# Optimization experiments

Hardware: AMD Instinct MI355X
Metric: run time of the kernel (lower is better)

Reference implementation:

```python
import jax, jax.numpy as jnp
import numpy as np

EMB_DIM = 1024
N_HEADS = 16
HEAD_DIM = EMB_DIM // N_HEADS
MAX_SEQ_LEN = 2048
THETA = 10000.0
B, T = 2, 2048


def _precompute_rope(head_dim, max_seq_len, theta=THETA):
    freqs = 1.0 / theta ** (np.arange(0, head_dim, 2, dtype=np.float32) / head_dim)
    t = np.arange(max_seq_len, dtype=np.float32)
    ang = np.outer(t, freqs)  # [T, D/2]
    return jnp.asarray(np.cos(ang)), jnp.asarray(np.sin(ang))


def setup_inputs() -> dict:
    key = jax.random.key(0)
    kx, kqkv, kp, kb = jax.random.split(key, 4)
    x = jax.random.normal(kx, (B, T, EMB_DIM), dtype=jnp.float32)
    # nn.Linear weights stored as [out, in]; we keep [in, out] for x @ W
    s1 = 1.0 / np.sqrt(EMB_DIM)
    Wqkv = jax.random.uniform(kqkv, (EMB_DIM, 3 * EMB_DIM), minval=-s1, maxval=s1, dtype=jnp.float32)
    Wproj = jax.random.uniform(kp, (EMB_DIM, EMB_DIM), minval=-s1, maxval=s1, dtype=jnp.float32)
    bproj = jax.random.uniform(kb, (EMB_DIM,), minval=-s1, maxval=s1, dtype=jnp.float32)
    cos, sin = _precompute_rope(HEAD_DIM, MAX_SEQ_LEN)
    return {"x": x, "Wqkv": Wqkv, "Wproj": Wproj, "bproj": bproj, "cos": cos, "sin": sin}


def _apply_rope(x, cos, sin):
    # x: [B,H,T,D]; cos/sin: [max_T, D/2]
    T_ = x.shape[-2]
    c, s = cos[:T_], sin[:T_]  # [T, D/2], broadcasts over B,H
    xe, xo = x[..., ::2], x[..., 1::2]
    re = xe * c - xo * s
    ro = xe * s + xo * c
    return jnp.stack([re, ro], axis=-1).reshape(x.shape)


def reference(x, Wqkv, Wproj, bproj, cos, sin):
    Bq, Tq, C = x.shape
    qkv = x @ Wqkv  # [B,T,3C]
    q, k, v = jnp.split(qkv, 3, axis=-1)
    def to_heads(t):
        return t.reshape(Bq, Tq, N_HEADS, HEAD_DIM).transpose(0, 2, 1, 3)  # [B,H,T,D]
    q, k, v = to_heads(q), to_heads(k), to_heads(v)
    q = _apply_rope(q, cos, sin)
    k = _apply_rope(k, cos, sin)
    scale = 1.0 / jnp.sqrt(jnp.asarray(HEAD_DIM, dtype=x.dtype))
    scores = jnp.einsum('bhqd,bhkd->bhqk', q, k) * scale  # [B,H,T,T]
    causal = jnp.tril(jnp.ones((Tq, Tq), dtype=bool))
    scores = jnp.where(causal, scores, jnp.asarray(-jnp.inf, dtype=scores.dtype))
    attn = jax.nn.softmax(scores, axis=-1)
    out = jnp.einsum('bhqk,bhkd->bhqd', attn, v)  # [B,H,T,D]
    out = out.transpose(0, 2, 1, 3).reshape(Bq, Tq, C)
    return out @ Wproj + bproj
```

## Files before the change

kernel.cpp:

```cpp
#include <hip/hip_runtime.h>

typedef __attribute__((ext_vector_type(8))) short short8;
typedef __attribute__((ext_vector_type(4))) float f32x4;
typedef __attribute__((ext_vector_type(4))) unsigned short u16x4;
typedef unsigned short ushort_t;

#define GLOAD16(gp, sp) __builtin_amdgcn_global_load_lds( \
    (const __attribute__((address_space(1))) void*)(gp),  \
    (__attribute__((address_space(3))) void*)(sp), 16, 0, 0)

#define MFMA(a, b, c) __builtin_amdgcn_mfma_f32_16x16x32_bf16(a, b, c, 0, 0, 0)

__device__ __forceinline__ ushort_t f2b(float f) {
    union { float f; unsigned u; } c; c.f = f;
    unsigned r = (c.u + 0x7FFFu + ((c.u >> 16) & 1u)) >> 16;
    return (ushort_t)r;
}
__device__ __forceinline__ float b2f(ushort_t u) {
    union { unsigned u; float f; } c; c.u = ((unsigned)u) << 16;
    return c.f;
}

__global__ void cvt_bf16(const float* __restrict__ in, ushort_t* __restrict__ out, int n) {
    int i = (blockIdx.x * 256 + threadIdx.x) * 4;
    if (i < n) {
        f32x4 v = *(const f32x4*)(in + i);
        u16x4 o;
        #pragma unroll
        for (int j = 0; j < 4; j++) o[j] = f2b(v[j]);
        *(u16x4*)(out + i) = o;
    }
}

__global__ __launch_bounds__(256) void transpose_cvt(const float* __restrict__ in,
                                                     ushort_t* __restrict__ out,
                                                     int R, int Cc) {
    __shared__ float tile[32][33];
    int tx = threadIdx.x & 31, ty = threadIdx.x >> 5;
    int c0 = blockIdx.x * 32, r0 = blockIdx.y * 32;
    #pragma unroll
    for (int i = 0; i < 32; i += 8)
        tile[ty + i][tx] = in[(size_t)(r0 + ty + i) * Cc + c0 + tx];
    __syncthreads();
    #pragma unroll
    for (int i = 0; i < 32; i += 8)
        out[(size_t)(c0 + ty + i) * R + r0 + tx] = f2b(tile[tx][ty + i]);
}

template <bool F32OUT, bool BIAS>
__global__ __launch_bounds__(256) void gemm_bt(const ushort_t* __restrict__ A,
                                               const ushort_t* __restrict__ Bt,
                                               void* __restrict__ Cout,
                                               const float* __restrict__ bias,
                                               int M, int N, int K) {
    __shared__ ushort_t lA[2][128 * 32];
    __shared__ ushort_t lB[2][128 * 32];
    const int tid = threadIdx.x;
    const int l = tid & 63, wv = tid >> 6;
    const int g = l >> 4, q16 = l & 15;
    const int m0 = blockIdx.y * 128, n0 = blockIdx.x * 128;
    const int wr = wv >> 1, wc = wv & 1;

    f32x4 acc[4][4];
    #pragma unroll
    for (int i = 0; i < 4; i++)
        #pragma unroll
        for (int j = 0; j < 4; j++) acc[i][j] = (f32x4){0.f, 0.f, 0.f, 0.f};

    const ushort_t* ga = A + (size_t)(m0 + wv * 32 + (l >> 2)) * K + (l & 3) * 8;
    const ushort_t* gb = Bt + (size_t)(n0 + wv * 32 + (l >> 2)) * K + (l & 3) * 8;

#define GSTAGE(buf_, k0_) do {                                                 \
    GLOAD16(ga + (k0_),                 &lA[buf_][wv * 1024]);                 \
    GLOAD16(ga + (k0_) + (size_t)16 * K, &lA[buf_][wv * 1024 + 512]);          \
    GLOAD16(gb + (k0_),                 &lB[buf_][wv * 1024]);                 \
    GLOAD16(gb + (k0_) + (size_t)16 * K, &lB[buf_][wv * 1024 + 512]);          \
} while (0)

    const int nt = K >> 5;
    GSTAGE(0, 0);
    __syncthreads();

    for (int t = 0; t < nt; ++t) {
        const int cur = t & 1;
        if (t + 1 < nt) GSTAGE(cur ^ 1, (t + 1) << 5);

        const ushort_t* sa = lA[cur];
        const ushort_t* sb = lB[cur];
        short8 af[4], bf[4];
        #pragma unroll
        for (int mi = 0; mi < 4; mi++)
            af[mi] = *(const short8*)(sa + (wr * 64 + mi * 16 + q16) * 32 + g * 8);
        #pragma unroll
        for (int ni = 0; ni < 4; ni++)
            bf[ni] = *(const short8*)(sb + (wc * 64 + ni * 16 + q16) * 32 + g * 8);
        #pragma unroll
        for (int mi = 0; mi < 4; mi++)
            #pragma unroll
            for (int ni = 0; ni < 4; ni++)
                acc[mi][ni] = MFMA(af[mi], bf[ni], acc[mi][ni]);

        __syncthreads();
    }

    #pragma unroll
    for (int ni = 0; ni < 4; ni++) {
        const int n = n0 + wc * 64 + ni * 16 + q16;
        float bv = 0.f;
        if (BIAS) bv = bias[n];
        #pragma unroll
        for (int mi = 0; mi < 4; mi++) {
            const int mbase = m0 + wr * 64 + mi * 16 + g * 4;
            #pragma unroll
            for (int r = 0; r < 4; r++) {
                if (F32OUT) {
                    ((float*)Cout)[(size_t)(mbase + r) * N + n] = acc[mi][ni][r] + bv;
                } else {
                    ((ushort_t*)Cout)[(size_t)(mbase + r) * N + n] = f2b(acc[mi][ni][r]);
                }
            }
        }
    }
#undef GSTAGE
}

__global__ void rope_scatter(const ushort_t* __restrict__ qkv,
                             const float* __restrict__ cosT, const float* __restrict__ sinT,
                             ushort_t* __restrict__ Qr, ushort_t* __restrict__ Kr,
                             ushort_t* __restrict__ Vt) {
    const float QS = 0.1803368801f;
    int tid = blockIdx.x * 256 + threadIdx.x;
    {
        int dc = tid & 7;
        int bht = tid >> 3;
        int t = bht & 2047, bh = bht >> 11;
        int b = bh >> 4, h = bh & 15;
        size_t mrow = ((size_t)b * 2048 + t) * 3072;
        short8 qv = *(const short8*)(qkv + mrow + h * 64 + dc * 8);
        short8 kv = *(const short8*)(qkv + mrow + 1024 + h * 64 + dc * 8);
        f32x4 cv = *(const f32x4*)(cosT + t * 32 + dc * 4);
        f32x4 sv = *(const f32x4*)(sinT + t * 32 + dc * 4);
        short8 qo, ko;
        #pragma unroll
        for (int j = 0; j < 4; j++) {
            float qe = b2f((ushort_t)qv[2 * j]), qod = b2f((ushort_t)qv[2 * j + 1]);
            float ke = b2f((ushort_t)kv[2 * j]), kod = b2f((ushort_t)kv[2 * j + 1]);
            qo[2 * j]     = (short)f2b((qe * cv[j] - qod * sv[j]) * QS);
            qo[2 * j + 1] = (short)f2b((qe * sv[j] + qod * cv[j]) * QS);
            ko[2 * j]     = (short)f2b(ke * cv[j] - kod * sv[j]);
            ko[2 * j + 1] = (short)f2b(ke * sv[j] + kod * cv[j]);
        }
        *(short8*)(Qr + ((size_t)bh * 2048 + t) * 64 + dc * 8) = qo;
        *(short8*)(Kr + ((size_t)bh * 2048 + t) * 64 + dc * 8) = ko;
    }
    {
        int t = tid & 2047;
        int rest = tid >> 11;
        int dc = rest & 7, bh = rest >> 3;
        int b = bh >> 4, h = bh & 15;
        const ushort_t* vs = qkv + ((size_t)b * 2048 + t) * 3072 + 2048 + h * 64 + dc * 8;
        int tp = (t & ~31) + ((t & 12) << 1) + ((t & 16) >> 2) + (t & 3);
        #pragma unroll
        for (int j = 0; j < 8; j++)
            Vt[((size_t)bh * 64 + dc * 8 + j) * 2048 + tp] = vs[j];
    }
}


__device__ __forceinline__ void tile64(
    const f32x4& S0, const f32x4& S1, const f32x4& S2, const f32x4& S3,
    int qpos, bool msk, int kvb, int g, float& ls,
    f32x4& o0, f32x4& o1, f32x4& o2, f32x4& o3,
    const short8& va0, const short8& va1, const short8& va2, const short8& va3,
    const short8& vb0, const short8& vb1, const short8& vb2, const short8& vb3) {
    float sv[16];
    #pragma unroll
    for (int r = 0; r < 4; r++) {
        sv[r] = S0[r]; sv[4 + r] = S1[r]; sv[8 + r] = S2[r]; sv[12 + r] = S3[r];
    }
    if (msk) {
        int kb0 = kvb + (g << 2);
        #pragma unroll
        for (int G = 0; G < 4; G++)
            #pragma unroll
            for (int r = 0; r < 4; r++)
                if (kb0 + 16 * G + r > qpos) sv[G * 4 + r] = -INFINITY;
    }
    float pp[16];
    #pragma unroll
    for (int i = 0; i < 16; i++) pp[i] = __builtin_amdgcn_exp2f(sv[i]);
    ls += (((pp[0] + pp[1]) + (pp[2] + pp[3])) + ((pp[4] + pp[5]) + (pp[6] + pp[7]))) +
          (((pp[8] + pp[9]) + (pp[10] + pp[11])) + ((pp[12] + pp[13]) + (pp[14] + pp[15])));
    union { short8 s; unsigned u[4]; } p0, p1;
    asm("v_cvt_pk_bf16_f32 %0, %1, %2" : "=v"(p0.u[0]) : "v"(pp[0]), "v"(pp[1]));
    asm("v_cvt_pk_bf16_f32 %0, %1, %2" : "=v"(p0.u[1]) : "v"(pp[2]), "v"(pp[3]));
    asm("v_cvt_pk_bf16_f32 %0, %1, %2" : "=v"(p0.u[2]) : "v"(pp[4]), "v"(pp[5]));
    asm("v_cvt_pk_bf16_f32 %0, %1, %2" : "=v"(p0.u[3]) : "v"(pp[6]), "v"(pp[7]));
    asm("v_cvt_pk_bf16_f32 %0, %1, %2" : "=v"(p1.u[0]) : "v"(pp[8]), "v"(pp[9]));
    asm("v_cvt_pk_bf16_f32 %0, %1, %2" : "=v"(p1.u[1]) : "v"(pp[10]), "v"(pp[11]));
    asm("v_cvt_pk_bf16_f32 %0, %1, %2" : "=v"(p1.u[2]) : "v"(pp[12]), "v"(pp[13]));
    asm("v_cvt_pk_bf16_f32 %0, %1, %2" : "=v"(p1.u[3]) : "v"(pp[14]), "v"(pp[15]));
    o0 = MFMA(va0, p0.s, o0); o0 = MFMA(vb0, p1.s, o0);
    o1 = MFMA(va1, p0.s, o1); o1 = MFMA(vb1, p1.s, o1);
    o2 = MFMA(va2, p0.s, o2); o2 = MFMA(vb2, p1.s, o2);
    o3 = MFMA(va3, p0.s, o3); o3 = MFMA(vb3, p1.s, o3);
}

#define EPI(LS, O0, O1, O2, O3, QPOS) do {                                     \
    float l2_ = LS + __shfl_xor(LS, 16);                                       \
    l2_ += __shfl_xor(l2_, 32);                                                \
    float ri_ = 1.0f / l2_;                                                    \
    ushort_t* op_ = Aout + ((size_t)(bq * 2048 + (QPOS)) << 10) + (h << 6) + (g << 2); \
    u16x4 o_;                                                                  \
    o_[0] = f2b(O0[0] * ri_); o_[1] = f2b(O0[1] * ri_);                        \
    o_[2] = f2b(O0[2] * ri_); o_[3] = f2b(O0[3] * ri_);                        \
    *(u16x4*)op_ = o_;                                                         \
    o_[0] = f2b(O1[0] * ri_); o_[1] = f2b(O1[1] * ri_);                        \
    o_[2] = f2b(O1[2] * ri_); o_[3] = f2b(O1[3] * ri_);                        \
    *(u16x4*)(op_ + 16) = o_;                                                  \
    o_[0] = f2b(O2[0] * ri_); o_[1] = f2b(O2[1] * ri_);                        \
    o_[2] = f2b(O2[2] * ri_); o_[3] = f2b(O2[3] * ri_);                        \
    *(u16x4*)(op_ + 32) = o_;                                                  \
    o_[0] = f2b(O3[0] * ri_); o_[1] = f2b(O3[1] * ri_);                        \
    o_[2] = f2b(O3[2] * ri_); o_[3] = f2b(O3[3] * ri_);                        \
    *(u16x4*)(op_ + 48) = o_;                                                  \
} while (0)

__global__ __launch_bounds__(256, 2) void attn_fwd(const ushort_t* __restrict__ Qr,
                                                   const ushort_t* __restrict__ Kr,
                                                   const ushort_t* __restrict__ Vt,
                                                   ushort_t* __restrict__ Aout) {
    __shared__ __attribute__((aligned(16))) ushort_t Ksh[2][4096];
    __shared__ __attribute__((aligned(16))) ushort_t Vsh[2][4096];

    const int tid = threadIdx.x;
    const int l = tid & 63, wv = tid >> 6;
    const int g = l >> 4, q16 = l & 15;
    const int xcd = blockIdx.x & 7, loc = blockIdx.x >> 3;
    const int h2 = loc >> 4;
    const int bh = (xcd << 2) | h2;
    int slot = loc & 15;
    if (h2 & 2) slot = 15 - slot;
    const int p = slot * 4 + wv;
    const int qlo = p << 4, qhi = (127 - p) << 4;
    const int qpos_l = qlo + q16, qpos_h = qhi + q16;
    const int bq = bh >> 4, h = bh & 15;

    const int ntot_bk = (((127 - slot * 4) << 4) + 79) >> 6;
    const int ntot_w  = (qhi + 79) >> 6;
    const int nlo_w   = (qlo + 79) >> 6;

    const ushort_t* Qp = Qr + ((size_t)bh * 2048) * 64;
    short8 ql0 = *(const short8*)(Qp + (size_t)qpos_l * 64 + g * 8);
    short8 ql1 = *(const short8*)(Qp + (size_t)qpos_l * 64 + g * 8 + 32);
    short8 qh0 = *(const short8*)(Qp + (size_t)qpos_h * 64 + g * 8);
    short8 qh1 = *(const short8*)(Qp + (size_t)qpos_h * 64 + g * 8 + 32);

    const ushort_t* Kb = Kr + (size_t)bh * 2048 * 64;
    const ushort_t* Vb = Vt + (size_t)bh * 64 * 2048;

    const ushort_t* ksrcA = Kb + (size_t)(wv * 16 + (l >> 3)) * 64 + (((l & 7) ^ (l >> 3)) << 3);
    const ushort_t* vsrcA = Vb + (size_t)(wv * 16 + (l >> 2)) * 2048 + (((l & 3) ^ ((l >> 3) & 3)) << 3);

#define STAGE(buf_, t_) do {                                                   \
    const ushort_t* ka_ = ksrcA + (size_t)(t_) * 4096;                         \
    const ushort_t* va_ = vsrcA + (t_) * 64;                                   \
    GLOAD16(ka_,       &Ksh[buf_][wv * 1024]);                                 \
    GLOAD16(ka_ + 512, &Ksh[buf_][wv * 1024 + 512]);                           \
    GLOAD16(va_,       &Vsh[buf_][wv * 512]);                                  \
    GLOAD16(va_ + 32,  &Vsh[buf_][2048 + wv * 512]);                           \
} while (0)

    const int kx  = q16 & 7;
    const int kq  = q16 * 128;
    const int kh0 = (g ^ kx) << 4;
    const int kh1 = ((g + 4) ^ kx) << 4;
    const int vsw = (g ^ ((q16 >> 1) & 3)) << 4;
    const int vq  = q16 * 64;

    float ls_l = 0.f, ls_h = 0.f;
    f32x4 ol0 = {0.f,0.f,0.f,0.f}, ol1 = {0.f,0.f,0.f,0.f};
    f32x4 ol2 = {0.f,0.f,0.f,0.f}, ol3 = {0.f,0.f,0.f,0.f};
    f32x4 oh0 = {0.f,0.f,0.f,0.f}, oh1 = {0.f,0.f,0.f,0.f};
    f32x4 oh2 = {0.f,0.f,0.f,0.f}, oh3 = {0.f,0.f,0.f,0.f};

    STAGE(0, 0);
    __syncthreads();

    for (int t = 0; t < ntot_bk; ++t) {
        const int nxt = t + 1;
        if (nxt < ntot_bk) {
            if (nxt & 1) STAGE(1, nxt); else STAGE(0, nxt);
        }
        if (t < ntot_w) {
            const char* Kc = (const char*)(t & 1 ? Ksh[1] : Ksh[0]);
            const char* Vc = (const char*)(t & 1 ? Vsh[1] : Vsh[0]);
            short8 k00 = *(const short8*)(Kc + kq + kh0);
            short8 k01 = *(const short8*)(Kc + kq + kh1);
            short8 k10 = *(const short8*)(Kc + kq + 2048 + kh0);
            short8 k11 = *(const short8*)(Kc + kq + 2048 + kh1);
            short8 k20 = *(const short8*)(Kc + kq + 4096 + kh0);
            short8 k21 = *(const short8*)(Kc + kq + 4096 + kh1);
            short8 k30 = *(const short8*)(Kc + kq + 6144 + kh0);
            short8 k31 = *(const short8*)(Kc + kq + 6144 + kh1);
            f32x4 s0 = {0.f,0.f,0.f,0.f}, s1 = {0.f,0.f,0.f,0.f};
            f32x4 s2 = {0.f,0.f,0.f,0.f}, s3 = {0.f,0.f,0.f,0.f};
            s0 = MFMA(k00, qh0, s0); s0 = MFMA(k01, qh1, s0);
            s1 = MFMA(k10, qh0, s1); s1 = MFMA(k11, qh1, s1);
            s2 = MFMA(k20, qh0, s2); s2 = MFMA(k21, qh1, s2);
            s3 = MFMA(k30, qh0, s3); s3 = MFMA(k31, qh1, s3);
            const bool lo_on = t < nlo_w;
            f32x4 u0 = {0.f,0.f,0.f,0.f}, u1 = {0.f,0.f,0.f,0.f};
            f32x4 u2 = {0.f,0.f,0.f,0.f}, u3 = {0.f,0.f,0.f,0.f};
            if (lo_on) {
                u0 = MFMA(k00, ql0, u0); u0 = MFMA(k01, ql1, u0);
                u1 = MFMA(k10, ql0, u1); u1 = MFMA(k11, ql1, u1);
                u2 = MFMA(k20, ql0, u2); u2 = MFMA(k21, ql1, u2);
                u3 = MFMA(k30, ql0, u3); u3 = MFMA(k31, ql1, u3);
            }
            short8 va0 = *(const short8*)(Vc + vq + vsw);
            short8 va1 = *(const short8*)(Vc + vq + 1024 + vsw);
            short8 va2 = *(const short8*)(Vc + vq + 2048 + vsw);
            short8 va3 = *(const short8*)(Vc + vq + 3072 + vsw);
            short8 vb0 = *(const short8*)(Vc + 4096 + vq + vsw);
            short8 vb1 = *(const short8*)(Vc + 4096 + vq + 1024 + vsw);
            short8 vb2 = *(const short8*)(Vc + 4096 + vq + 2048 + vsw);
            short8 vb3 = *(const short8*)(Vc + 4096 + vq + 3072 + vsw);
            const int kvb = t << 6;
            tile64(s0, s1, s2, s3, qpos_h, kvb + 63 > qhi, kvb, g, ls_h,
                   oh0, oh1, oh2, oh3, va0, va1, va2, va3, vb0, vb1, vb2, vb3);
            if (lo_on)
                tile64(u0, u1, u2, u3, qpos_l, kvb + 63 > qlo, kvb, g, ls_l,
                       ol0, ol1, ol2, ol3, va0, va1, va2, va3, vb0, vb1, vb2, vb3);
        }
        __syncthreads();
    }

    EPI(ls_l, ol0, ol1, ol2, ol3, qpos_l);
    EPI(ls_h, oh0, oh1, oh2, oh3, qpos_h);
#undef STAGE
}

extern "C" void kernel_launch(void* const* d_in, const int* in_sizes, int n_in,
                              void* d_out, int out_size, void* d_ws, size_t ws_size,
                              hipStream_t stream) {
    const float* x     = (const float*)d_in[0];
    const float* Wqkv  = (const float*)d_in[1];
    const float* Wproj = (const float*)d_in[2];
    const float* bproj = (const float*)d_in[3];
    const float* cosT  = (const float*)d_in[4];
    const float* sinT  = (const float*)d_in[5];

    char* ws = (char*)d_ws;
    ushort_t* xb     = (ushort_t*)(ws);
    ushort_t* WqkvT  = (ushort_t*)(ws + (8u  << 20));
    ushort_t* WprojT = (ushort_t*)(ws + (14u << 20));
    ushort_t* qkv    = (ushort_t*)(ws + (16u << 20));
    ushort_t* Qr     = (ushort_t*)(ws + (40u << 20));
    ushort_t* Kr     = (ushort_t*)(ws + (48u << 20));
    ushort_t* Vt     = (ushort_t*)(ws + (56u << 20));
    ushort_t* aout   = (ushort_t*)(ws + (64u << 20));

    cvt_bf16<<<4096, 256, 0, stream>>>(x, xb, 4096 * 1024);
    transpose_cvt<<<dim3(96, 32), 256, 0, stream>>>(Wqkv, WqkvT, 1024, 3072);
    transpose_cvt<<<dim3(32, 32), 256, 0, stream>>>(Wproj, WprojT, 1024, 1024);

    gemm_bt<false, false><<<dim3(24, 32), 256, 0, stream>>>(xb, WqkvT, (void*)qkv, nullptr,
                                                            4096, 3072, 1024);
    rope_scatter<<<2048, 256, 0, stream>>>(qkv, cosT, sinT, Qr, Kr, Vt);
    attn_fwd<<<512, 256, 0, stream>>>(Qr, Kr, Vt, aout);
    gemm_bt<true, true><<<dim3(8, 32), 256, 0, stream>>>(aout, WprojT, d_out, bproj,
                                                         4096, 1024, 1024);
}
```

Measured before the change: 186.3 us.

## Triple-buffer GEMM LDS staging and remap blocks to XCDs for locality

The GEMM's LDS pipeline grows from double to triple buffering, prefetching two K-tiles ahead. Each step waits with explicit vmcnt counts and a raw s_barrier instead of a full __syncthreads, so load latency is hidden longer. The launch grid is flattened to 1D and block indices are remapped so each XCD gets a contiguous band of M-rows, improving L2 reuse of the A tiles. The cost is more shared memory per block, which may reduce occupancy, plus hand-tuned waitcnt logic that is fragile if the load count changes.

```diff
diff --git a/kernel.cpp b/kernel.cpp
--- a/kernel.cpp
+++ b/kernel.cpp
@@ -47,18 +47,25 @@
         out[(size_t)(c0 + ty + i) * R + r0 + tx] = f2b(tile[tx][ty + i]);
 }
 
+#define WAITV4 asm volatile("s_waitcnt vmcnt(4)" ::: "memory")
+#define WAITV0 asm volatile("s_waitcnt vmcnt(0)" ::: "memory")
+#define SBAR do { __builtin_amdgcn_s_barrier(); __builtin_amdgcn_sched_barrier(0); } while (0)
+
 template <bool F32OUT, bool BIAS>
 __global__ __launch_bounds__(256) void gemm_bt(const ushort_t* __restrict__ A,
                                                const ushort_t* __restrict__ Bt,
                                                void* __restrict__ Cout,
                                                const float* __restrict__ bias,
-                                               int M, int N, int K) {
-    __shared__ ushort_t lA[2][128 * 32];
-    __shared__ ushort_t lB[2][128 * 32];
+                                               int M, int N, int K, int nx) {
+    __shared__ ushort_t lA[3][4096];
+    __shared__ ushort_t lB[3][4096];
     const int tid = threadIdx.x;
     const int l = tid & 63, wv = tid >> 6;
     const int g = l >> 4, q16 = l & 15;
-    const int m0 = blockIdx.y * 128, n0 = blockIdx.x * 128;
+    const int xcd = blockIdx.x & 7, idx = blockIdx.x >> 3;
+    const int ry = (int)(gridDim.x >> 3) / nx;
+    const int m0 = (xcd * ry + idx / nx) * 128;
+    const int n0 = (idx % nx) * 128;
     const int wr = wv >> 1, wc = wv & 1;
 
     f32x4 acc[4][4];
@@ -71,19 +78,21 @@
     const ushort_t* gb = Bt + (size_t)(n0 + wv * 32 + (l >> 2)) * K + (l & 3) * 8;
 
 #define GSTAGE(buf_, k0_) do {                                                 \
-    GLOAD16(ga + (k0_),                 &lA[buf_][wv * 1024]);                 \
+    GLOAD16(ga + (k0_),                  &lA[buf_][wv * 1024]);                \
     GLOAD16(ga + (k0_) + (size_t)16 * K, &lA[buf_][wv * 1024 + 512]);          \
-    GLOAD16(gb + (k0_),                 &lB[buf_][wv * 1024]);                 \
+    GLOAD16(gb + (k0_),                  &lB[buf_][wv * 1024]);                \
     GLOAD16(gb + (k0_) + (size_t)16 * K, &lB[buf_][wv * 1024 + 512]);          \
 } while (0)
 
     const int nt = K >> 5;
     GSTAGE(0, 0);
-    __syncthreads();
-
-    for (int t = 0; t < nt; ++t) {
-        const int cur = t & 1;
-        if (t + 1 < nt) GSTAGE(cur ^ 1, (t + 1) << 5);
+    GSTAGE(1, 32);
+    WAITV4;
+    SBAR;
+
+    for (int t = 0, cur = 0; t < nt; ++t) {
+        int stg = cur + 2; if (stg >= 3) stg -= 3;
+        if (t + 2 < nt) GSTAGE(stg, (t + 2) << 5);
 
         const ushort_t* sa = lA[cur];
         const ushort_t* sb = lB[cur];
@@ -100,7 +109,11 @@
             for (int ni = 0; ni < 4; ni++)
                 acc[mi][ni] = MFMA(af[mi], bf[ni], acc[mi][ni]);
 
-        __syncthreads();
+        if (t + 1 < nt) {
+            if (t + 2 < nt) { WAITV4; } else { WAITV0; }
+            SBAR;
+        }
+        ++cur; if (cur == 3) cur = 0;
     }
 
     #pragma unroll
@@ -365,10 +378,10 @@
     transpose_cvt<<<dim3(96, 32), 256, 0, stream>>>(Wqkv, WqkvT, 1024, 3072);
     transpose_cvt<<<dim3(32, 32), 256, 0, stream>>>(Wproj, WprojT, 1024, 1024);
 
-    gemm_bt<false, false><<<dim3(24, 32), 256, 0, stream>>>(xb, WqkvT, (void*)qkv, nullptr,
-                                                            4096, 3072, 1024);
+    gemm_bt<false, false><<<768, 256, 0, stream>>>(xb, WqkvT, (void*)qkv, nullptr,
+                                                   4096, 3072, 1024, 24);
     rope_scatter<<<2048, 256, 0, stream>>>(qkv, cosT, sinT, Qr, Kr, Vt);
     attn_fwd<<<512, 256, 0, stream>>>(Qr, Kr, Vt, aout);
-    gemm_bt<true, true><<<dim3(8, 32), 256, 0, stream>>>(aout, WprojT, d_out, bproj,
-                                                         4096, 1024, 1024);
-}
+    gemm_bt<true, true><<<256, 256, 0, stream>>>(aout, WprojT, d_out, bproj,
+                                                 4096, 1024, 1024, 8);
+}
```

Result: no change. 187.0 us (+0.4%).
